# Kernel tuning notes

Hardware: AMD Instinct MI355X
Metric: run time of the kernel (lower is better)

## Reference

```python
import jax, jax.numpy as jnp
import numpy as np

WIN = (8, 8)
HEADS = 16
DIM = 512
HEAD_DIM = DIM // HEADS
SCALE = HEAD_DIM ** -0.5


def _rel_pos_index(wh, ww):
    # same construction as the torch buffer relative_position_index
    coords = np.stack(np.meshgrid(np.arange(wh), np.arange(ww), indexing='ij'))  # (2, wh, ww)
    cf = coords.reshape(2, -1)                      # (2, N)
    rel = cf[:, :, None] - cf[:, None, :]           # (2, N, N)
    rel = rel.transpose(1, 2, 0).astype(np.int64)   # (N, N, 2)
    rel[..., 0] += wh - 1
    rel[..., 1] += ww - 1
    rel[..., 0] *= 2 * ww - 1
    return rel.sum(-1)                              # (N, N)


def setup_inputs() -> dict:
    key = jax.random.key(0)
    ks = jax.random.split(key, 6)
    B = 1024
    x = jax.random.normal(ks[0], (B, DIM, WIN[0], WIN[1]), dtype=jnp.float32)
    # torch Linear uses W of shape (out,in); we store (in,out) and matmul directly.
    Wq = jax.random.normal(ks[1], (DIM, DIM), dtype=jnp.float32) * (DIM ** -0.5)
    bq = jnp.zeros((DIM,), dtype=jnp.float32)
    Wkv = jax.random.normal(ks[2], (DIM, 2 * DIM), dtype=jnp.float32) * (DIM ** -0.5)
    bkv = jnp.zeros((2 * DIM,), dtype=jnp.float32)
    bias_table = jax.random.normal(ks[3], ((2 * WIN[0] - 1) * (2 * WIN[1] - 1), HEADS), dtype=jnp.float32) * 0.02
    w_blend = jnp.ones((2,), dtype=jnp.float32)
    Wp = jax.random.normal(ks[4], (DIM, DIM), dtype=jnp.float32) * (DIM ** -0.5)
    bp = jnp.zeros((DIM,), dtype=jnp.float32)
    return {"x": x, "Wq": Wq, "bq": bq, "Wkv": Wkv, "bkv": bkv,
            "bias_table": bias_table, "w_blend": w_blend, "Wp": Wp, "bp": bp}


def reference(x, Wq, bq, Wkv, bkv, bias_table, w_blend, Wp, bp):
    B, C, h, w = x.shape
    N = h * w
    xf = x.reshape(B, C, N).transpose(0, 2, 1)                      # (B, N, C)

    q = (xf @ Wq + bq).reshape(B, N, HEADS, HEAD_DIM).transpose(0, 2, 1, 3)
    kv = xf @ Wkv + bkv                                             # (B, N, 2C)
    k = kv[..., :C].reshape(B, N, HEADS, HEAD_DIM).transpose(0, 2, 1, 3)
    v = kv[..., C:].reshape(B, N, HEADS, HEAD_DIM).transpose(0, 2, 1, 3)

    attn = jnp.einsum('bhnd,bhmd->bhnm', q * SCALE, k)              # (B, H, N, N)

    rpi = jnp.asarray(_rel_pos_index(*WIN))                         # (N, N)
    bias = bias_table[rpi].transpose(2, 0, 1)                       # (H, N, N)
    attn = attn + bias[None]

    attn0 = jax.nn.softmax(attn, axis=-1)
    attn1 = jnp.square(jnp.maximum(attn, 0.0))
    wts = jax.nn.softmax(w_blend)
    a = attn0 * wts[0] + attn1 * wts[1]

    out = jnp.einsum('bhnm,bhmd->bhnd', a, v)                       # (B, H, N, D)
    out = out.transpose(0, 2, 1, 3).reshape(B, N, C)
    out = out @ Wp + bp
    return out.transpose(0, 2, 1).reshape(B, C, h, w)
```

## Files before the change

### kernel.cpp

```cpp
#include <hip/hip_runtime.h>

typedef unsigned short ushort_t;
typedef __attribute__((ext_vector_type(4))) float f32x4;
typedef __attribute__((ext_vector_type(8))) short bf16x8;
typedef __attribute__((ext_vector_type(4))) unsigned short u16x4;

#define MFMA(a, b, c) __builtin_amdgcn_mfma_f32_16x16x32_bf16((a), (b), (c), 0, 0, 0)

__device__ __forceinline__ unsigned short f2bf(float f) {
    unsigned int u = __builtin_bit_cast(unsigned int, f);
    u += 0x7fffu + ((u >> 16) & 1u);
    return (unsigned short)(u >> 16);
}
__device__ __forceinline__ float bf2f(unsigned short h) {
    unsigned int u = ((unsigned int)h) << 16;
    return __builtin_bit_cast(float, u);
}
__device__ __forceinline__ void split2(float f, unsigned short& h, unsigned short& l) {
    h = f2bf(f);
    l = f2bf(f - bf2f(h));
}

__device__ __forceinline__ void gload16(const void* g, void* l) {
    __builtin_amdgcn_global_load_lds(
        (const __attribute__((address_space(1))) void*)g,
        (__attribute__((address_space(3))) void*)l, 16, 0, 0);
}

__global__ __launch_bounds__(256) void wsplit_kernel(const float* __restrict__ W,
                                                     ushort_t* __restrict__ Thi,
                                                     ushort_t* __restrict__ Tlo,
                                                     int K, int N) {
    __shared__ float tile[64][65];
    int nb = N >> 6;
    int bx = blockIdx.x % nb;
    int by = blockIdx.x / nb;
    int n0 = bx * 64, k0 = by * 64;
    int t = threadIdx.x;
    int c4 = (t & 15) * 4;
    int rr = t >> 4;
    #pragma unroll
    for (int i = 0; i < 4; ++i) {
        int r = rr + i * 16;
        f32x4 vv = *(const f32x4*)(W + (size_t)(k0 + r) * N + n0 + c4);
        tile[r][c4 + 0] = vv[0];
        tile[r][c4 + 1] = vv[1];
        tile[r][c4 + 2] = vv[2];
        tile[r][c4 + 3] = vv[3];
    }
    __syncthreads();
    #pragma unroll
    for (int i = 0; i < 4; ++i) {
        int rn = rr + i * 16;
        u16x4 hv, lv;
        #pragma unroll
        for (int r2 = 0; r2 < 4; ++r2) {
            unsigned short hh, ll;
            split2(tile[c4 + r2][rn], hh, ll);
            hv[r2] = hh;
            lv[r2] = ll;
        }
        *(u16x4*)(Thi + (size_t)(n0 + rn) * K + k0 + c4) = hv;
        *(u16x4*)(Tlo + (size_t)(n0 + rn) * K + k0 + c4) = lv;
    }
}

__global__ __launch_bounds__(256) void xsplit_kernel(const float* __restrict__ x,
                                                     ushort_t* __restrict__ Thi,
                                                     ushort_t* __restrict__ Tlo) {
    __shared__ float tile[64][65];
    int b = blockIdx.x >> 3;
    int k0 = (blockIdx.x & 7) * 64;
    const float* W = x + (size_t)b * 32768;
    ushort_t* Th = Thi + (size_t)b * 32768;
    ushort_t* Tl = Tlo + (size_t)b * 32768;
    int t = threadIdx.x;
    int c4 = (t & 15) * 4;
    int rr = t >> 4;
    #pragma unroll
    for (int i = 0; i < 4; ++i) {
        int r = rr + i * 16;
        f32x4 vv = *(const f32x4*)(W + (size_t)(k0 + r) * 64 + c4);
        tile[r][c4 + 0] = vv[0];
        tile[r][c4 + 1] = vv[1];
        tile[r][c4 + 2] = vv[2];
        tile[r][c4 + 3] = vv[3];
    }
    __syncthreads();
    #pragma unroll
    for (int i = 0; i < 4; ++i) {
        int rn = rr + i * 16;
        u16x4 hv, lv;
        #pragma unroll
        for (int r2 = 0; r2 < 4; ++r2) {
            unsigned short hh, ll;
            split2(tile[c4 + r2][rn], hh, ll);
            hv[r2] = hh;
            lv[r2] = ll;
        }
        *(u16x4*)(Th + (size_t)rn * 512 + k0 + c4) = hv;
        *(u16x4*)(Tl + (size_t)rn * 512 + k0 + c4) = lv;
    }
}

__global__ __launch_bounds__(256) void biasM_kernel(const float* __restrict__ table,
                                                    float* __restrict__ biasM) {
    int u = blockIdx.x * 256 + threadIdx.x;
    int h = u >> 12;
    int n = (u >> 6) & 63;
    int m = u & 63;
    int idx = ((n >> 3) - (m >> 3) + 7) * 15 + ((n & 7) - (m & 7) + 7);
    biasM[u] = table[idx * 16 + h];
}

__device__ __forceinline__ void stage_tile(const ushort_t* __restrict__ src,
                                           int rbase, int k0, char* lds, int t) {
    #pragma unroll
    for (int c = 0; c < 4; ++c) {
        int row = c * 32 + (t >> 3);
        int kb = ((t & 7) * 16) ^ ((row & 7) << 4);
        const ushort_t* g = src + (size_t)(rbase + row) * 512 + k0 + (kb >> 1);
        gload16(g, lds + c * 4096 + t * 16);
    }
}

__global__ __launch_bounds__(256, 2) void qkv_gemm(
    const ushort_t* __restrict__ xTh, const ushort_t* __restrict__ xTl,
    const ushort_t* __restrict__ BTh, const ushort_t* __restrict__ BTl,
    const float* __restrict__ bq, const float* __restrict__ bkv,
    ushort_t* __restrict__ qph, ushort_t* __restrict__ qpl,
    ushort_t* __restrict__ kph, ushort_t* __restrict__ kpl,
    ushort_t* __restrict__ vph, ushort_t* __restrict__ vpl,
    int gm) {
    extern __shared__ char sm[];
    char* As_h = sm;
    char* As_l = sm + 16384;
    char* Bs_h = sm + 32768;
    char* Bs_l = sm + 49152;

    int nb = gm * 12;
    int qq = nb >> 3, r8 = nb & 7;
    int xcd = blockIdx.x & 7, pos = blockIdx.x >> 3;
    int wg = (xcd < r8 ? xcd * (qq + 1) : r8 * (qq + 1) + (xcd - r8) * qq) + pos;
    int nt = wg / gm;
    int mt = wg - nt * gm;
    const int m0 = mt * 128;
    const int n0 = nt * 128;

    const int t = threadIdx.x;
    const int l = t & 63;
    const int w = t >> 6;
    const int ln = l & 15;
    const int g = l >> 4;
    const int wm = w >> 1;
    const int wn = w & 1;

    f32x4 acc[4][4];
    #pragma unroll
    for (int i = 0; i < 4; ++i)
        #pragma unroll
        for (int j = 0; j < 4; ++j) acc[i][j] = {0.f, 0.f, 0.f, 0.f};

    for (int ks = 0; ks < 8; ++ks) {
        const int k0 = ks * 64;
        stage_tile(xTh, m0, k0, As_h, t);
        stage_tile(xTl, m0, k0, As_l, t);
        stage_tile(BTh, n0, k0, Bs_h, t);
        stage_tile(BTl, n0, k0, Bs_l, t);
        __syncthreads();
        #pragma unroll
        for (int kf = 0; kf < 2; ++kf) {
            const int kb = kf * 64 + g * 16;
            bf16x8 Ah[4], Al[4];
            #pragma unroll
            for (int fi = 0; fi < 4; ++fi) {
                int row = wm * 64 + fi * 16 + ln;
                int off = row * 128 + (kb ^ ((row & 7) << 4));
                Ah[fi] = *(const bf16x8*)(As_h + off);
                Al[fi] = *(const bf16x8*)(As_l + off);
            }
            #pragma unroll
            for (int fj = 0; fj < 4; ++fj) {
                int cl = wn * 64 + fj * 16 + ln;
                int off = cl * 128 + (kb ^ ((cl & 7) << 4));
                bf16x8 Bh = *(const bf16x8*)(Bs_h + off);
                bf16x8 Bl = *(const bf16x8*)(Bs_l + off);
                #pragma unroll
                for (int fi = 0; fi < 4; ++fi) {
                    acc[fi][fj] = MFMA(Ah[fi], Bh, acc[fi][fj]);
                    acc[fi][fj] = MFMA(Ah[fi], Bl, acc[fi][fj]);
                    acc[fi][fj] = MFMA(Al[fi], Bh, acc[fi][fj]);
                }
            }
        }
        __syncthreads();
    }

    const int g4 = g * 4;
    #pragma unroll
    for (int fj = 0; fj < 4; ++fj) {
        int col = n0 + wn * 64 + fj * 16 + ln;
        int which = col >> 9;
        float bias = (which == 0) ? bq[col] : bkv[col - 512];
        float scl = (which == 0) ? 0.17677669529663689f : 1.f;
        int head = (col >> 5) & 15;
        int d = col & 31;
        ushort_t* ph = (which == 0) ? qph : (which == 1) ? kph : vph;
        ushort_t* pl = (which == 0) ? qpl : (which == 1) ? kpl : vpl;
        #pragma unroll
        for (int fi = 0; fi < 4; ++fi) {
            #pragma unroll
            for (int r = 0; r < 4; ++r) {
                int m = m0 + wm * 64 + fi * 16 + g4 + r;
                size_t off = (((size_t)(m >> 6) * 16 + head) * 64 + (m & 63)) * 32 + d;
                unsigned short hh, ll;
                split2((acc[fi][fj][r] + bias) * scl, hh, ll);
                ph[off] = hh;
                pl[off] = ll;
            }
        }
    }
}

__global__ __launch_bounds__(512, 4) void attn_kernel(
    const ushort_t* __restrict__ qph, const ushort_t* __restrict__ qpl,
    const ushort_t* __restrict__ kph, const ushort_t* __restrict__ kpl,
    const ushort_t* __restrict__ vph, const ushort_t* __restrict__ vpl,
    const float* __restrict__ biasM, const float* __restrict__ wbl,
    const ushort_t* __restrict__ WpTh, const ushort_t* __restrict__ WpTl,
    const float* __restrict__ bp, float* __restrict__ out) {
    __shared__ char a_h[8192];
    __shared__ char a_l[8192];
    __shared__ char v_h[4096];
    __shared__ char v_l[4096];
    char* ao_h = a_h;
    char* ao_l = a_l;

    const int b = blockIdx.x;
    const int tid = threadIdx.x;
    const int l = tid & 63;
    const int w = tid >> 6;
    const int ln = l & 15;
    const int g = l >> 4;
    const int nt = w >> 1;
    const int nA = nt * 16 + ln;
    const int nC = nt * 16 + g * 4;
    const int dcol = (w & 1) * 16 + ln;
    const int swA = (nA & 7) << 4;

    float wb0 = wbl[0], wb1 = wbl[1];
    float wm = fmaxf(wb0, wb1);
    float e0 = __expf(wb0 - wm), e1 = __expf(wb1 - wm);
    float wt0 = e0 / (e0 + e1), wt1 = e1 / (e0 + e1);

    f32x4 acc[16];
    #pragma unroll
    for (int i = 0; i < 16; ++i) acc[i] = {0.f, 0.f, 0.f, 0.f};

    for (int h = 0; h < 16; ++h) {
        const size_t hb = (size_t)b * 16 + h;

        if (w < 4) {
            const ushort_t* qbh = qph + hb * 2048;
            const ushort_t* qbl = qpl + hb * 2048;
            const ushort_t* kbh = kph + hb * 2048;
            const ushort_t* kbl = kpl + hb * 2048;
            f32x4 sv[4];
            int offq = (w * 16 + ln) * 32 + g * 8;
            bf16x8 Qh = *(const bf16x8*)(qbh + offq);
            bf16x8 Ql = *(const bf16x8*)(qbl + offq);
            #pragma unroll
            for (int mt = 0; mt < 4; ++mt) {
                int offk = (mt * 16 + ln) * 32 + g * 8;
                bf16x8 Kh = *(const bf16x8*)(kbh + offk);
                bf16x8 Kl = *(const bf16x8*)(kbl + offk);
                f32x4 s = {0.f, 0.f, 0.f, 0.f};
                s = MFMA(Qh, Kh, s);
                s = MFMA(Qh, Kl, s);
                s = MFMA(Ql, Kh, s);
                sv[mt] = s;
            }
            const float* bM = biasM + h * 4096;
            #pragma unroll
            for (int r = 0; r < 4; ++r) {
                int n_ = w * 16 + g * 4 + r;
                #pragma unroll
                for (int mt = 0; mt < 4; ++mt)
                    sv[mt][r] += bM[n_ * 64 + mt * 16 + ln];
            }
            #pragma unroll
            for (int r = 0; r < 4; ++r) {
                int n_ = w * 16 + g * 4 + r;
                float mx = fmaxf(fmaxf(sv[0][r], sv[1][r]), fmaxf(sv[2][r], sv[3][r]));
                mx = fmaxf(mx, __shfl_xor(mx, 1));
                mx = fmaxf(mx, __shfl_xor(mx, 2));
                mx = fmaxf(mx, __shfl_xor(mx, 4));
                mx = fmaxf(mx, __shfl_xor(mx, 8));
                float ex[4];
                float sum = 0.f;
                #pragma unroll
                for (int mt = 0; mt < 4; ++mt) {
                    ex[mt] = __expf(sv[mt][r] - mx);
                    sum += ex[mt];
                }
                sum += __shfl_xor(sum, 1);
                sum += __shfl_xor(sum, 2);
                sum += __shfl_xor(sum, 4);
                sum += __shfl_xor(sum, 8);
                float rinv0 = wt0 / sum;
                #pragma unroll
                for (int mt = 0; mt < 4; ++mt) {
                    int m_ = mt * 16 + ln;
                    float rl = fmaxf(sv[mt][r], 0.f);
                    float aval = ex[mt] * rinv0 + wt1 * rl * rl;
                    unsigned short hh, ll;
                    split2(aval, hh, ll);
                    int aoff = n_ * 128 + ((2 * m_) ^ ((n_ & 7) << 4));
                    *(unsigned short*)(a_h + aoff) = hh;
                    *(unsigned short*)(a_l + aoff) = ll;
                }
            }
        } else {
            int t2 = tid - 256;
            bf16x8 vh8 = *(const bf16x8*)(vph + hb * 2048 + t2 * 8);
            bf16x8 vl8 = *(const bf16x8*)(vpl + hb * 2048 + t2 * 8);
            int tok = t2 >> 2;
            int d0 = (t2 & 3) * 8;
            #pragma unroll
            for (int j = 0; j < 8; ++j) {
                int d = d0 + j;
                int off = d * 128 + ((tok * 2) ^ ((d & 7) << 4));
                *(unsigned short*)(v_h + off) = (unsigned short)vh8[j];
                *(unsigned short*)(v_l + off) = (unsigned short)vl8[j];
            }
        }
        __syncthreads();

        f32x4 ao = {0.f, 0.f, 0.f, 0.f};
        {
            const int swV = (dcol & 7) << 4;
            #pragma unroll
            for (int ks = 0; ks < 2; ++ks) {
                int mo = 2 * (ks * 32 + g * 8);
                bf16x8 Aa = *(const bf16x8*)(a_h + nA * 128 + (mo ^ swA));
                bf16x8 Ab = *(const bf16x8*)(a_l + nA * 128 + (mo ^ swA));
                bf16x8 Vh = *(const bf16x8*)(v_h + dcol * 128 + (mo ^ swV));
                bf16x8 Vl = *(const bf16x8*)(v_l + dcol * 128 + (mo ^ swV));
                ao = MFMA(Aa, Vh, ao);
                ao = MFMA(Aa, Vl, ao);
                ao = MFMA(Ab, Vh, ao);
            }
        }
        __syncthreads();

        #pragma unroll
        for (int r = 0; r < 4; ++r) {
            unsigned short hh, ll;
            split2(ao[r], hh, ll);
            *(unsigned short*)(ao_h + (nC + r) * 80 + 2 * dcol) = hh;
            *(unsigned short*)(ao_l + (nC + r) * 80 + 2 * dcol) = ll;
        }
        __syncthreads();

        {
            bf16x8 Ah[4], Al[4];
            #pragma unroll
            for (int ntl = 0; ntl < 4; ++ntl) {
                int offa = (ntl * 16 + ln) * 80 + 16 * g;
                Ah[ntl] = *(const bf16x8*)(ao_h + offa);
                Al[ntl] = *(const bf16x8*)(ao_l + offa);
            }
            const ushort_t* ph = WpTh + (size_t)(w * 64 + ln) * 512 + h * 32 + g * 8;
            const ushort_t* pl = WpTl + (size_t)(w * 64 + ln) * 512 + h * 32 + g * 8;
            #pragma unroll
            for (int ctl = 0; ctl < 4; ++ctl) {
                bf16x8 Bh = *(const bf16x8*)(ph + (size_t)ctl * 8192);
                bf16x8 Bl = *(const bf16x8*)(pl + (size_t)ctl * 8192);
                #pragma unroll
                for (int ntl = 0; ntl < 4; ++ntl) {
                    acc[ctl * 4 + ntl] = MFMA(Ah[ntl], Bh, acc[ctl * 4 + ntl]);
                    acc[ctl * 4 + ntl] = MFMA(Ah[ntl], Bl, acc[ctl * 4 + ntl]);
                    acc[ctl * 4 + ntl] = MFMA(Al[ntl], Bh, acc[ctl * 4 + ntl]);
                }
            }
        }
        __syncthreads();
    }

    #pragma unroll
    for (int ctl = 0; ctl < 4; ++ctl) {
        int cout = w * 64 + ctl * 16 + ln;
        float bb = bp[cout];
        #pragma unroll
        for (int ntl = 0; ntl < 4; ++ntl) {
            f32x4 o;
            #pragma unroll
            for (int r = 0; r < 4; ++r) o[r] = acc[ctl * 4 + ntl][r] + bb;
            *(f32x4*)(out + ((size_t)b * 512 + cout) * 64 + ntl * 16 + g * 4) = o;
        }
    }
}

extern "C" void kernel_launch(void* const* d_in, const int* in_sizes, int n_in,
                              void* d_out, int out_size, void* d_ws, size_t ws_size,
                              hipStream_t stream) {
    const float* x = (const float*)d_in[0];
    const float* Wq = (const float*)d_in[1];
    const float* bq = (const float*)d_in[2];
    const float* Wkv = (const float*)d_in[3];
    const float* bkv = (const float*)d_in[4];
    const float* btab = (const float*)d_in[5];
    const float* wbl = (const float*)d_in[6];
    const float* Wp = (const float*)d_in[7];
    const float* bp = (const float*)d_in[8];
    float* out = (float*)d_out;

    char* ws = (char*)d_ws;
    ushort_t* BTh = (ushort_t*)(ws + 0);
    ushort_t* BTl = (ushort_t*)(ws + 1572864);
    ushort_t* WpTh = (ushort_t*)(ws + 3145728);
    ushort_t* WpTl = (ushort_t*)(ws + 3670016);
    float* biasM = (float*)(ws + 4194304);

    const size_t qbase = 4456448;
    const size_t perwin = 524288;
    int npass;
    if (ws_size >= qbase + 1024 * perwin) npass = 1;
    else if (ws_size >= qbase + 512 * perwin) npass = 2;
    else npass = 4;
    const int wpp = 1024 / npass;
    const size_t C = (size_t)wpp * 65536;
    ushort_t* xTh = (ushort_t*)(ws + qbase);
    ushort_t* xTl = (ushort_t*)(ws + qbase + C);
    ushort_t* qph = (ushort_t*)(ws + qbase + 2 * C);
    ushort_t* qpl = (ushort_t*)(ws + qbase + 3 * C);
    ushort_t* kph = (ushort_t*)(ws + qbase + 4 * C);
    ushort_t* kpl = (ushort_t*)(ws + qbase + 5 * C);
    ushort_t* vph = (ushort_t*)(ws + qbase + 6 * C);
    ushort_t* vpl = (ushort_t*)(ws + qbase + 7 * C);

    wsplit_kernel<<<64, 256, 0, stream>>>(Wq, BTh, BTl, 512, 512);
    wsplit_kernel<<<128, 256, 0, stream>>>(Wkv, BTh + (size_t)512 * 512,
                                           BTl + (size_t)512 * 512, 512, 1024);
    wsplit_kernel<<<64, 256, 0, stream>>>(Wp, WpTh, WpTl, 512, 512);
    biasM_kernel<<<256, 256, 0, stream>>>(btab, biasM);

    (void)hipFuncSetAttribute((const void*)qkv_gemm,
                              hipFuncAttributeMaxDynamicSharedMemorySize, 65536);

    const int gm = wpp / 2;
    for (int p = 0; p < npass; ++p) {
        xsplit_kernel<<<wpp * 8, 256, 0, stream>>>(x + (size_t)p * wpp * 32768,
                                                   xTh, xTl);
        qkv_gemm<<<gm * 12, 256, 65536, stream>>>(xTh, xTl, BTh, BTl, bq, bkv,
                                                  qph, qpl, kph, kpl, vph, vpl,
                                                  gm);
        attn_kernel<<<wpp, 512, 0, stream>>>(qph, qpl, kph, kpl, vph, vpl,
                                             biasM, wbl, WpTh, WpTl, bp,
                                             out + (size_t)p * wpp * 32768);
    }
}
```

Baseline: 1.175 ms.

## Split output projection into separate GEMM kernel and parallelize attention over head groups

Removes the per-head fused output projection from the attention kernel and moves it into a separate tiled proj_gemm that reads the attention output from a new bf16 hi/lo workspace buffer. The attention kernel now runs four heads per block with four times as many blocks, prefetches the next head's Q/K in registers, and loads V asynchronously into LDS. V is stored pre-transposed and swizzled by the QKV GEMM, so the transpose no longer happens in LDS. This trades an extra global round-trip of the attention output, plus a larger workspace requirement, for better parallelism and GEMM-efficient projection.

Result: faster. 1.007 ms (-14.3%).

```diff
diff --git a/kernel.cpp b/kernel.cpp
--- a/kernel.cpp
+++ b/kernel.cpp
@@ -212,7 +212,11 @@
             #pragma unroll
             for (int r = 0; r < 4; ++r) {
                 int m = m0 + wm * 64 + fi * 16 + g4 + r;
-                size_t off = (((size_t)(m >> 6) * 16 + head) * 64 + (m & 63)) * 32 + d;
+                int tok = m & 63;
+                size_t hb = (size_t)(m >> 6) * 16 + head;
+                size_t off = (which == 2)
+                    ? hb * 2048 + d * 64 + (tok ^ ((d & 7) << 3))
+                    : hb * 2048 + tok * 32 + d;
                 unsigned short hh, ll;
                 split2((acc[fi][fj][r] + bias) * scl, hh, ll);
                 ph[off] = hh;
@@ -222,123 +226,209 @@
     }
 }
 
-__global__ __launch_bounds__(512, 4) void attn_kernel(
+__global__ __launch_bounds__(256, 2) void proj_gemm(
+    const ushort_t* __restrict__ Ah_, const ushort_t* __restrict__ Al_,
+    const ushort_t* __restrict__ Bh_, const ushort_t* __restrict__ Bl_,
+    const float* __restrict__ bp, float* __restrict__ out, int gm) {
+    extern __shared__ char sm[];
+    char* As_h = sm;
+    char* As_l = sm + 16384;
+    char* Bs_h = sm + 32768;
+    char* Bs_l = sm + 49152;
+
+    int nb = gm * 4;
+    int qq = nb >> 3, r8 = nb & 7;
+    int xcd = blockIdx.x & 7, pos = blockIdx.x >> 3;
+    int wg = (xcd < r8 ? xcd * (qq + 1) : r8 * (qq + 1) + (xcd - r8) * qq) + pos;
+    int nt = wg / gm;
+    int mt = wg - nt * gm;
+    const int m0 = mt * 128;
+    const int n0 = nt * 128;
+
+    const int t = threadIdx.x;
+    const int l = t & 63;
+    const int w = t >> 6;
+    const int ln = l & 15;
+    const int g = l >> 4;
+    const int wm = w >> 1;
+    const int wn = w & 1;
+
+    f32x4 acc[4][4];
+    #pragma unroll
+    for (int i = 0; i < 4; ++i)
+        #pragma unroll
+        for (int j = 0; j < 4; ++j) acc[i][j] = {0.f, 0.f, 0.f, 0.f};
+
+    for (int ks = 0; ks < 8; ++ks) {
+        const int k0 = ks * 64;
+        stage_tile(Ah_, m0, k0, As_h, t);
+        stage_tile(Al_, m0, k0, As_l, t);
+        stage_tile(Bh_, n0, k0, Bs_h, t);
+        stage_tile(Bl_, n0, k0, Bs_l, t);
+        __syncthreads();
+        #pragma unroll
+        for (int kf = 0; kf < 2; ++kf) {
+            const int kb = kf * 64 + g * 16;
+            bf16x8 Ah[4], Al[4];
+            #pragma unroll
+            for (int fi = 0; fi < 4; ++fi) {
+                int row = wm * 64 + fi * 16 + ln;
+                int off = row * 128 + (kb ^ ((row & 7) << 4));
+                Ah[fi] = *(const bf16x8*)(As_h + off);
+                Al[fi] = *(const bf16x8*)(As_l + off);
+            }
+            #pragma unroll
+            for (int fj = 0; fj < 4; ++fj) {
+                int cl = wn * 64 + fj * 16 + ln;
+                int off = cl * 128 + (kb ^ ((cl & 7) << 4));
+                bf16x8 Bh = *(const bf16x8*)(Bs_h + off);
+                bf16x8 Bl = *(const bf16x8*)(Bs_l + off);
+                #pragma unroll
+                for (int fi = 0; fi < 4; ++fi) {
+                    acc[fi][fj] = MFMA(Ah[fi], Bh, acc[fi][fj]);
+                    acc[fi][fj] = MFMA(Ah[fi], Bl, acc[fi][fj]);
+                    acc[fi][fj] = MFMA(Al[fi], Bh, acc[fi][fj]);
+                }
+            }
+        }
+        __syncthreads();
+    }
+
+    const int g4 = g * 4;
+    #pragma unroll
+    for (int fj = 0; fj < 4; ++fj) {
+        int col = n0 + wn * 64 + fj * 16 + ln;
+        float bias = bp[col];
+        #pragma unroll
+        for (int fi = 0; fi < 4; ++fi) {
+            int m = m0 + wm * 64 + fi * 16 + g4;
+            f32x4 o;
+            #pragma unroll
+            for (int r = 0; r < 4; ++r) o[r] = acc[fi][fj][r] + bias;
+            *(f32x4*)(out + ((size_t)(m >> 6) * 512 + col) * 64 + (m & 63)) = o;
+        }
+    }
+}
+
+__global__ __launch_bounds__(256, 4) void attn_kernel(
     const ushort_t* __restrict__ qph, const ushort_t* __restrict__ qpl,
     const ushort_t* __restrict__ kph, const ushort_t* __restrict__ kpl,
     const ushort_t* __restrict__ vph, const ushort_t* __restrict__ vpl,
     const float* __restrict__ biasM, const float* __restrict__ wbl,
-    const ushort_t* __restrict__ WpTh, const ushort_t* __restrict__ WpTl,
-    const float* __restrict__ bp, float* __restrict__ out) {
+    ushort_t* __restrict__ aoPh, ushort_t* __restrict__ aoPl) {
     __shared__ char a_h[8192];
     __shared__ char a_l[8192];
     __shared__ char v_h[4096];
     __shared__ char v_l[4096];
-    char* ao_h = a_h;
-    char* ao_l = a_l;
-
-    const int b = blockIdx.x;
+
+    const int blk = blockIdx.x;
+    const int win = blk >> 2;
+    const int q0 = (blk & 3) << 2;
     const int tid = threadIdx.x;
     const int l = tid & 63;
     const int w = tid >> 6;
     const int ln = l & 15;
     const int g = l >> 4;
-    const int nt = w >> 1;
-    const int nA = nt * 16 + ln;
-    const int nC = nt * 16 + g * 4;
-    const int dcol = (w & 1) * 16 + ln;
+    const int nA = w * 16 + ln;
     const int swA = (nA & 7) << 4;
 
     float wb0 = wbl[0], wb1 = wbl[1];
-    float wm = fmaxf(wb0, wb1);
-    float e0 = __expf(wb0 - wm), e1 = __expf(wb1 - wm);
+    float wmx = fmaxf(wb0, wb1);
+    float e0 = __expf(wb0 - wmx), e1 = __expf(wb1 - wmx);
     float wt0 = e0 / (e0 + e1), wt1 = e1 / (e0 + e1);
 
-    f32x4 acc[16];
-    #pragma unroll
-    for (int i = 0; i < 16; ++i) acc[i] = {0.f, 0.f, 0.f, 0.f};
-
-    for (int h = 0; h < 16; ++h) {
-        const size_t hb = (size_t)b * 16 + h;
-
-        if (w < 4) {
-            const ushort_t* qbh = qph + hb * 2048;
-            const ushort_t* qbl = qpl + hb * 2048;
-            const ushort_t* kbh = kph + hb * 2048;
-            const ushort_t* kbl = kpl + hb * 2048;
-            f32x4 sv[4];
-            int offq = (w * 16 + ln) * 32 + g * 8;
-            bf16x8 Qh = *(const bf16x8*)(qbh + offq);
-            bf16x8 Ql = *(const bf16x8*)(qbl + offq);
+    const int offq = (w * 16 + ln) * 32 + g * 8;
+    const int offk = ln * 32 + g * 8;
+
+    size_t pb = ((size_t)win * 16 + q0) * 2048;
+    bf16x8 nQh = *(const bf16x8*)(qph + pb + offq);
+    bf16x8 nQl = *(const bf16x8*)(qpl + pb + offq);
+    bf16x8 nKh[4], nKl[4];
+    #pragma unroll
+    for (int mt = 0; mt < 4; ++mt) {
+        nKh[mt] = *(const bf16x8*)(kph + pb + offk + mt * 512);
+        nKl[mt] = *(const bf16x8*)(kpl + pb + offk + mt * 512);
+    }
+    gload16(vph + pb + tid * 8, v_h + tid * 16);
+    gload16(vpl + pb + tid * 8, v_l + tid * 16);
+
+    #pragma unroll
+    for (int hh = 0; hh < 4; ++hh) {
+        const int h = q0 + hh;
+        bf16x8 Qh = nQh, Ql = nQl;
+        bf16x8 Kh[4], Kl[4];
+        #pragma unroll
+        for (int mt = 0; mt < 4; ++mt) { Kh[mt] = nKh[mt]; Kl[mt] = nKl[mt]; }
+
+        f32x4 sv[4];
+        #pragma unroll
+        for (int mt = 0; mt < 4; ++mt) {
+            f32x4 s = {0.f, 0.f, 0.f, 0.f};
+            s = MFMA(Qh, Kh[mt], s);
+            s = MFMA(Qh, Kl[mt], s);
+            s = MFMA(Ql, Kh[mt], s);
+            sv[mt] = s;
+        }
+
+        if (hh < 3) {
+            size_t pn = ((size_t)win * 16 + h + 1) * 2048;
+            nQh = *(const bf16x8*)(qph + pn + offq);
+            nQl = *(const bf16x8*)(qpl + pn + offq);
             #pragma unroll
             for (int mt = 0; mt < 4; ++mt) {
-                int offk = (mt * 16 + ln) * 32 + g * 8;
-                bf16x8 Kh = *(const bf16x8*)(kbh + offk);
-                bf16x8 Kl = *(const bf16x8*)(kbl + offk);
-                f32x4 s = {0.f, 0.f, 0.f, 0.f};
-                s = MFMA(Qh, Kh, s);
-                s = MFMA(Qh, Kl, s);
-                s = MFMA(Ql, Kh, s);
-                sv[mt] = s;
-            }
-            const float* bM = biasM + h * 4096;
-            #pragma unroll
-            for (int r = 0; r < 4; ++r) {
-                int n_ = w * 16 + g * 4 + r;
-                #pragma unroll
-                for (int mt = 0; mt < 4; ++mt)
-                    sv[mt][r] += bM[n_ * 64 + mt * 16 + ln];
-            }
-            #pragma unroll
-            for (int r = 0; r < 4; ++r) {
-                int n_ = w * 16 + g * 4 + r;
-                float mx = fmaxf(fmaxf(sv[0][r], sv[1][r]), fmaxf(sv[2][r], sv[3][r]));
-                mx = fmaxf(mx, __shfl_xor(mx, 1));
-                mx = fmaxf(mx, __shfl_xor(mx, 2));
-                mx = fmaxf(mx, __shfl_xor(mx, 4));
-                mx = fmaxf(mx, __shfl_xor(mx, 8));
-                float ex[4];
-                float sum = 0.f;
-                #pragma unroll
-                for (int mt = 0; mt < 4; ++mt) {
-                    ex[mt] = __expf(sv[mt][r] - mx);
-                    sum += ex[mt];
-                }
-                sum += __shfl_xor(sum, 1);
-                sum += __shfl_xor(sum, 2);
-                sum += __shfl_xor(sum, 4);
-                sum += __shfl_xor(sum, 8);
-                float rinv0 = wt0 / sum;
-                #pragma unroll
-                for (int mt = 0; mt < 4; ++mt) {
-                    int m_ = mt * 16 + ln;
-                    float rl = fmaxf(sv[mt][r], 0.f);
-                    float aval = ex[mt] * rinv0 + wt1 * rl * rl;
-                    unsigned short hh, ll;
-                    split2(aval, hh, ll);
-                    int aoff = n_ * 128 + ((2 * m_) ^ ((n_ & 7) << 4));
-                    *(unsigned short*)(a_h + aoff) = hh;
-                    *(unsigned short*)(a_l + aoff) = ll;
-                }
-            }
-        } else {
-            int t2 = tid - 256;
-            bf16x8 vh8 = *(const bf16x8*)(vph + hb * 2048 + t2 * 8);
-            bf16x8 vl8 = *(const bf16x8*)(vpl + hb * 2048 + t2 * 8);
-            int tok = t2 >> 2;
-            int d0 = (t2 & 3) * 8;
-            #pragma unroll
-            for (int j = 0; j < 8; ++j) {
-                int d = d0 + j;
-                int off = d * 128 + ((tok * 2) ^ ((d & 7) << 4));
-                *(unsigned short*)(v_h + off) = (unsigned short)vh8[j];
-                *(unsigned short*)(v_l + off) = (unsigned short)vl8[j];
+                nKh[mt] = *(const bf16x8*)(kph + pn + offk + mt * 512);
+                nKl[mt] = *(const bf16x8*)(kpl + pn + offk + mt * 512);
+            }
+        }
+
+        const float* bM = biasM + h * 4096;
+        #pragma unroll
+        for (int r = 0; r < 4; ++r) {
+            int n_ = w * 16 + g * 4 + r;
+            #pragma unroll
+            for (int mt = 0; mt < 4; ++mt)
+                sv[mt][r] += bM[n_ * 64 + mt * 16 + ln];
+        }
+        #pragma unroll
+        for (int r = 0; r < 4; ++r) {
+            int n_ = w * 16 + g * 4 + r;
+            float mx = fmaxf(fmaxf(sv[0][r], sv[1][r]), fmaxf(sv[2][r], sv[3][r]));
+            mx = fmaxf(mx, __shfl_xor(mx, 1));
+            mx = fmaxf(mx, __shfl_xor(mx, 2));
+            mx = fmaxf(mx, __shfl_xor(mx, 4));
+            mx = fmaxf(mx, __shfl_xor(mx, 8));
+            float ex[4];
+            float sum = 0.f;
+            #pragma unroll
+            for (int mt = 0; mt < 4; ++mt) {
+                ex[mt] = __expf(sv[mt][r] - mx);
+                sum += ex[mt];
+            }
+            sum += __shfl_xor(sum, 1);
+            sum += __shfl_xor(sum, 2);
+            sum += __shfl_xor(sum, 4);
+            sum += __shfl_xor(sum, 8);
+            float rinv0 = wt0 / sum;
+            #pragma unroll
+            for (int mt = 0; mt < 4; ++mt) {
+                int m_ = mt * 16 + ln;
+                float rl = fmaxf(sv[mt][r], 0.f);
+                float aval = ex[mt] * rinv0 + wt1 * rl * rl;
+                unsigned short hv, lv;
+                split2(aval, hv, lv);
+                int aoff = n_ * 128 + ((2 * m_) ^ ((n_ & 7) << 4));
+                *(unsigned short*)(a_h + aoff) = hv;
+                *(unsigned short*)(a_l + aoff) = lv;
             }
         }
         __syncthreads();
 
-        f32x4 ao = {0.f, 0.f, 0.f, 0.f};
-        {
+        f32x4 ao[2];
+        #pragma unroll
+        for (int dt = 0; dt < 2; ++dt) {
+            const int dcol = dt * 16 + ln;
             const int swV = (dcol & 7) << 4;
+            f32x4 o = {0.f, 0.f, 0.f, 0.f};
             #pragma unroll
             for (int ks = 0; ks < 2; ++ks) {
                 int mo = 2 * (ks * 32 + g * 8);
@@ -346,57 +436,31 @@
                 bf16x8 Ab = *(const bf16x8*)(a_l + nA * 128 + (mo ^ swA));
                 bf16x8 Vh = *(const bf16x8*)(v_h + dcol * 128 + (mo ^ swV));
                 bf16x8 Vl = *(const bf16x8*)(v_l + dcol * 128 + (mo ^ swV));
-                ao = MFMA(Aa, Vh, ao);
-                ao = MFMA(Aa, Vl, ao);
-                ao = MFMA(Ab, Vh, ao);
-            }
+                o = MFMA(Aa, Vh, o);
+                o = MFMA(Aa, Vl, o);
+                o = MFMA(Ab, Vh, o);
+            }
+            ao[dt] = o;
         }
         __syncthreads();
 
-        #pragma unroll
-        for (int r = 0; r < 4; ++r) {
-            unsigned short hh, ll;
-            split2(ao[r], hh, ll);
-            *(unsigned short*)(ao_h + (nC + r) * 80 + 2 * dcol) = hh;
-            *(unsigned short*)(ao_l + (nC + r) * 80 + 2 * dcol) = ll;
-        }
-        __syncthreads();
-
-        {
-            bf16x8 Ah[4], Al[4];
-            #pragma unroll
-            for (int ntl = 0; ntl < 4; ++ntl) {
-                int offa = (ntl * 16 + ln) * 80 + 16 * g;
-                Ah[ntl] = *(const bf16x8*)(ao_h + offa);
-                Al[ntl] = *(const bf16x8*)(ao_l + offa);
-            }
-            const ushort_t* ph = WpTh + (size_t)(w * 64 + ln) * 512 + h * 32 + g * 8;
-            const ushort_t* pl = WpTl + (size_t)(w * 64 + ln) * 512 + h * 32 + g * 8;
-            #pragma unroll
-            for (int ctl = 0; ctl < 4; ++ctl) {
-                bf16x8 Bh = *(const bf16x8*)(ph + (size_t)ctl * 8192);
-                bf16x8 Bl = *(const bf16x8*)(pl + (size_t)ctl * 8192);
-                #pragma unroll
-                for (int ntl = 0; ntl < 4; ++ntl) {
-                    acc[ctl * 4 + ntl] = MFMA(Ah[ntl], Bh, acc[ctl * 4 + ntl]);
-                    acc[ctl * 4 + ntl] = MFMA(Ah[ntl], Bl, acc[ctl * 4 + ntl]);
-                    acc[ctl * 4 + ntl] = MFMA(Al[ntl], Bh, acc[ctl * 4 + ntl]);
-                }
-            }
-        }
-        __syncthreads();
-    }
-
-    #pragma unroll
-    for (int ctl = 0; ctl < 4; ++ctl) {
-        int cout = w * 64 + ctl * 16 + ln;
-        float bb = bp[cout];
-        #pragma unroll
-        for (int ntl = 0; ntl < 4; ++ntl) {
-            f32x4 o;
-            #pragma unroll
-            for (int r = 0; r < 4; ++r) o[r] = acc[ctl * 4 + ntl][r] + bb;
-            *(f32x4*)(out + ((size_t)b * 512 + cout) * 64 + ntl * 16 + g * 4) = o;
+        if (hh < 3) {
+            size_t pn = ((size_t)win * 16 + h + 1) * 2048;
+            gload16(vph + pn + tid * 8, v_h + tid * 16);
+            gload16(vpl + pn + tid * 8, v_l + tid * 16);
+        }
+
+        #pragma unroll
+        for (int dt = 0; dt < 2; ++dt) {
+            #pragma unroll
+            for (int r = 0; r < 4; ++r) {
+                int n_ = w * 16 + g * 4 + r;
+                size_t o = ((size_t)win * 64 + n_) * 512 + h * 32 + dt * 16 + ln;
+                unsigned short hv, lv;
+                split2(ao[dt][r], hv, lv);
+                aoPh[o] = hv;
+                aoPl[o] = lv;
+            }
         }
     }
 }
@@ -423,10 +487,9 @@
     float* biasM = (float*)(ws + 4194304);
 
     const size_t qbase = 4456448;
-    const size_t perwin = 524288;
     int npass;
-    if (ws_size >= qbase + 1024 * perwin) npass = 1;
-    else if (ws_size >= qbase + 512 * perwin) npass = 2;
+    if (ws_size >= qbase + (size_t)1024 * 655360) npass = 1;
+    else if (ws_size >= qbase + (size_t)512 * 655360) npass = 2;
     else npass = 4;
     const int wpp = 1024 / npass;
     const size_t C = (size_t)wpp * 65536;
@@ -438,6 +501,8 @@
     ushort_t* kpl = (ushort_t*)(ws + qbase + 5 * C);
     ushort_t* vph = (ushort_t*)(ws + qbase + 6 * C);
     ushort_t* vpl = (ushort_t*)(ws + qbase + 7 * C);
+    ushort_t* aoPh = (ushort_t*)(ws + qbase + 8 * C);
+    ushort_t* aoPl = (ushort_t*)(ws + qbase + 9 * C);
 
     wsplit_kernel<<<64, 256, 0, stream>>>(Wq, BTh, BTl, 512, 512);
     wsplit_kernel<<<128, 256, 0, stream>>>(Wkv, BTh + (size_t)512 * 512,
@@ -446,6 +511,8 @@
     biasM_kernel<<<256, 256, 0, stream>>>(btab, biasM);
 
     (void)hipFuncSetAttribute((const void*)qkv_gemm,
+                              hipFuncAttributeMaxDynamicSharedMemorySize, 65536);
+    (void)hipFuncSetAttribute((const void*)proj_gemm,
                               hipFuncAttributeMaxDynamicSharedMemorySize, 65536);
 
     const int gm = wpp / 2;
@@ -455,8 +522,10 @@
         qkv_gemm<<<gm * 12, 256, 65536, stream>>>(xTh, xTl, BTh, BTl, bq, bkv,
                                                   qph, qpl, kph, kpl, vph, vpl,
                                                   gm);
-        attn_kernel<<<wpp, 512, 0, stream>>>(qph, qpl, kph, kpl, vph, vpl,
-                                             biasM, wbl, WpTh, WpTl, bp,
-                                             out + (size_t)p * wpp * 32768);
-    }
-}
+        attn_kernel<<<wpp * 4, 256, 0, stream>>>(qph, qpl, kph, kpl, vph, vpl,
+                                                 biasM, wbl, aoPh, aoPl);
+        proj_gemm<<<gm * 4, 256, 65536, stream>>>(aoPh, aoPl, WpTh, WpTl, bp,
+                                                  out + (size_t)p * wpp * 32768,
+                                                  gm);
+    }
+}
```
